# Performance work log

Hardware: AMD Instinct MI355X
Metric: run time of the kernel (lower is better)

The kernel has to match this reference:

```python
import jax, jax.numpy as jnp
import numpy as np

# Model constants (match init_kwargs and fla GatedLinearAttention defaults used in source)
L = 4            # num_layers
D = 1024         # d_model
H = 4            # n_heads
DK = 128         # head key dim  = 0.5*D / H
DV = 256         # head value dim = 1.0*D / H
KD = H * DK      # total key dim = 512
VD = H * DV      # total value dim = 1024
V = 32000        # vocab
B, T = 1, 2048
LR = 16          # gate_low_rank_dim
GLN = 16.0       # gate_logit_normalizer
EPS = 1e-5
SCALE = DK ** -0.5


def setup_inputs() -> dict:
    key = jax.random.key(0)
    ks = jax.random.split(key, 12)
    s = 0.02
    return {
        "input_ids": jax.random.randint(ks[0], (B, T), 0, V),
        "emb": jax.random.normal(ks[1], (V, D), jnp.float32) * s,
        "Wq": jax.random.normal(ks[2], (L, D, KD), jnp.float32) * s,
        "Wk": jax.random.normal(ks[3], (L, D, KD), jnp.float32) * s,
        "Wv": jax.random.normal(ks[4], (L, D, VD), jnp.float32) * s,
        "Wg": jax.random.normal(ks[5], (L, D, VD), jnp.float32) * s,
        "Wgk1": jax.random.normal(ks[6], (L, D, LR), jnp.float32) * s,
        "Wgk2": jax.random.normal(ks[7], (L, LR, KD), jnp.float32) * s,
        "bgk": jnp.zeros((L, KD), jnp.float32),
        "gnw": jnp.ones((L, DV), jnp.float32),
        "Wo": jax.random.normal(ks[8], (L, VD, D), jnp.float32) * s,
        "ln_w": jnp.ones((D,), jnp.float32),
        "ln_b": jnp.zeros((D,), jnp.float32),
        "Wlm": jax.random.normal(ks[9], (D, V), jnp.float32) * s,
        "blm": jnp.zeros((V,), jnp.float32),
    }


def _gla_layer(x, wq, wk, wv, wg, wg1, wg2, bg, nw, wo):
    # x: [B, T, D]
    b, t, _ = x.shape
    q = (x @ wq).reshape(b, t, H, DK) * SCALE
    k = (x @ wk).reshape(b, t, H, DK)
    v = (x @ wv).reshape(b, t, H, DV)
    g = (x @ wg).reshape(b, t, H, DV)
    # low-rank forget gate, log-space, normalized
    gk = (jax.nn.log_sigmoid((x @ wg1) @ wg2 + bg) / GLN).reshape(b, t, H, DK)

    # time-major for scan: [T, B, H, *]
    qt, kt, vt, gkt = (jnp.moveaxis(a, 1, 0) for a in (q, k, v, gk))

    def step(S, inp):
        q_t, k_t, v_t, gk_t = inp  # [B,H,DK], [B,H,DK], [B,H,DV], [B,H,DK]
        S = S * jnp.exp(gk_t)[..., None] + k_t[..., None] * v_t[..., None, :]
        o_t = jnp.einsum('bhk,bhkv->bhv', q_t, S)
        return S, o_t

    S0 = jnp.zeros((b, H, DK, DV), x.dtype)
    _, o = jax.lax.scan(step, S0, (qt, kt, vt, gkt))
    o = jnp.moveaxis(o, 0, 1)  # [B, T, H, DV]
    # fused RMSNorm + swish output gate
    o = o * jax.lax.rsqrt(jnp.mean(o * o, axis=-1, keepdims=True) + EPS) * nw
    o = o * (g * jax.nn.sigmoid(g))
    return o.reshape(b, t, VD) @ wo


def reference(input_ids, emb, Wq, Wk, Wv, Wg, Wgk1, Wgk2, bgk, gnw, Wo, ln_w, ln_b, Wlm, blm):
    h = emb[input_ids]  # [B, T, D]
    for i in range(L):
        h = _gla_layer(h, Wq[i], Wk[i], Wv[i], Wg[i], Wgk1[i], Wgk2[i], bgk[i], gnw[i], Wo[i])
    mu = jnp.mean(h, axis=-1, keepdims=True)
    var = jnp.mean((h - mu) ** 2, axis=-1, keepdims=True)
    h = (h - mu) * jax.lax.rsqrt(var + EPS) * ln_w + ln_b
    return h @ Wlm + blm
```

## Files before the change

kernel.cpp:

```cpp
#include <hip/hip_runtime.h>
#include <hip/hip_bf16.h>
#include <math.h>

#define NL 4
#define TT 2048
#define DD 1024
#define KDIM 512
#define VDIM 1024
#define QSTR 3072
#define NH 4
#define DKH 128
#define DVH 256
#define CH 64
#define NCH 32
#define VOCAB 32000
#define SCALE_Q 0.08838834764831845f

typedef short bf16x8 __attribute__((ext_vector_type(8)));
typedef float f32x4 __attribute__((ext_vector_type(4)));

__device__ __forceinline__ void gload_lds16(const void* g, void* l) {
    __builtin_amdgcn_global_load_lds((const __attribute__((address_space(1))) void*)g,
                                     (__attribute__((address_space(3))) void*)l, 16, 0, 0);
}

__device__ __forceinline__ void store_bf16x4(__hip_bfloat16* p, float a, float b, float c, float d) {
    union { __hip_bfloat16 h[4]; ushort4 v; } r;
    r.h[0] = __float2bfloat16(a); r.h[1] = __float2bfloat16(b);
    r.h[2] = __float2bfloat16(c); r.h[3] = __float2bfloat16(d);
    *(ushort4*)p = r.v;
}

__global__ __launch_bounds__(256) void embed_kernel(const int* __restrict__ ids,
                                                    const float* __restrict__ emb,
                                                    float* __restrict__ h,
                                                    __hip_bfloat16* __restrict__ hb) {
    int idx = blockIdx.x * 256 + threadIdx.x;
    int t = idx >> 8, c4 = idx & 255;
    float4 v = *(const float4*)(emb + (size_t)ids[t] * DD + c4 * 4);
    *(float4*)(h + (size_t)t * DD + c4 * 4) = v;
    store_bf16x4(hb + (size_t)t * DD + c4 * 4, v.x, v.y, v.z, v.w);
}

__global__ __launch_bounds__(256) void tconv_kernel(const float* __restrict__ in,
                                                    __hip_bfloat16* __restrict__ out,
                                                    int K, int N) {
    __shared__ float tle[64][65];
    const int n0 = blockIdx.x * 64, k0 = blockIdx.y * 64;
    const int tid = threadIdx.x;
    const int ty = tid >> 4, tx = tid & 15;
#pragma unroll
    for (int u = 0; u < 4; u++) {
        int r = ty + u * 16;
        float4 v = *(const float4*)(in + (size_t)(k0 + r) * N + n0 + tx * 4);
        tle[r][tx * 4 + 0] = v.x; tle[r][tx * 4 + 1] = v.y;
        tle[r][tx * 4 + 2] = v.z; tle[r][tx * 4 + 3] = v.w;
    }
    __syncthreads();
#pragma unroll
    for (int u = 0; u < 4; u++) {
        int nn = u * 16 + ty;
        store_bf16x4(out + (size_t)(n0 + nn) * K + k0 + tx * 4,
                     tle[tx * 4 + 0][nn], tle[tx * 4 + 1][nn],
                     tle[tx * 4 + 2][nn], tle[tx * 4 + 3][nn]);
    }
}

__global__ __launch_bounds__(256) void tconv_all_kernel(const float* __restrict__ Wq,
                                                        const float* __restrict__ Wk,
                                                        const float* __restrict__ Wv,
                                                        const float* __restrict__ Wg,
                                                        const float* __restrict__ Wo,
                                                        __hip_bfloat16* __restrict__ Wt4,
                                                        __hip_bfloat16* __restrict__ WoT4) {
    __shared__ float tle[64][65];
    int l = blockIdx.x >> 10;
    int b = blockIdx.x & 1023;
    const float* wq = Wq + (size_t)l * DD * KDIM;
    const float* wk = Wk + (size_t)l * DD * KDIM;
    const float* wv = Wv + (size_t)l * DD * VDIM;
    const float* wg = Wg + (size_t)l * DD * VDIM;
    const float* wo = Wo + (size_t)l * VDIM * DD;
    __hip_bfloat16* Wt  = Wt4  + (size_t)l * QSTR * DD;
    __hip_bfloat16* WoT = WoT4 + (size_t)l * DD * VDIM;
    const float* src; __hip_bfloat16* dst; int N, local;
    if (b < 128)      { src = wq; dst = Wt;                         N = 512;  local = b; }
    else if (b < 256) { src = wk; dst = Wt + (size_t)512 * 1024;    N = 512;  local = b - 128; }
    else if (b < 512) { src = wv; dst = Wt + (size_t)1024 * 1024;   N = 1024; local = b - 256; }
    else if (b < 768) { src = wg; dst = Wt + (size_t)2048 * 1024;   N = 1024; local = b - 512; }
    else              { src = wo; dst = WoT;                        N = 1024; local = b - 768; }
    int nbx = N >> 6;
    int n0 = (local % nbx) * 64, k0 = (local / nbx) * 64;
    const int tid = threadIdx.x;
    const int ty = tid >> 4, tx = tid & 15;
#pragma unroll
    for (int u = 0; u < 4; u++) {
        int r = ty + u * 16;
        float4 v = *(const float4*)(src + (size_t)(k0 + r) * N + n0 + tx * 4);
        tle[r][tx * 4 + 0] = v.x; tle[r][tx * 4 + 1] = v.y;
        tle[r][tx * 4 + 2] = v.z; tle[r][tx * 4 + 3] = v.w;
    }
    __syncthreads();
#pragma unroll
    for (int u = 0; u < 4; u++) {
        int nn = u * 16 + ty;
        store_bf16x4(dst + (size_t)(n0 + nn) * 1024 + k0 + tx * 4,
                     tle[tx * 4 + 0][nn], tle[tx * 4 + 1][nn],
                     tle[tx * 4 + 2][nn], tle[tx * 4 + 3][nn]);
    }
}

template<int NF>
__global__ __launch_bounds__(256) void gemm_bf16_db(const __hip_bfloat16* __restrict__ A,
                                                    const __hip_bfloat16* __restrict__ Bt,
                                                    const float* __restrict__ bias,
                                                    float* __restrict__ C,
                                                    __hip_bfloat16* __restrict__ Cb,
                                                    int M, int N, int K) {
    __shared__ short a_lds[2][128 * 32];
    __shared__ short b_lds[2][NF * 32 * 32];
    const int tid = threadIdx.x;
    const int wv = tid >> 6, lane = tid & 63;
    const int wr = wv >> 1, wc = wv & 1;
    const int nbx = gridDim.x;
    int wg = blockIdx.y * nbx + blockIdx.x;
    int cpx = (nbx * gridDim.y) >> 3;
    int swz = (wg & 7) * cpx + (wg >> 3);
    const int m0 = (swz % nbx) * 128, n0 = (swz / nbx) * (NF * 32);
    const int lr = lane & 15, lk = (lane >> 4) * 8;

    f32x4 acc[4][NF];
#pragma unroll
    for (int m = 0; m < 4; m++)
#pragma unroll
        for (int n = 0; n < NF; n++) acc[m][n] = (f32x4)(0.f);

    auto STAGE = [&](int buf, int k0) {
#pragma unroll
        for (int u = 0; u < 2; u++) {
            int s = wv * 128 + u * 64 + lane;
            int r = s >> 2, kc = (s & 3) * 8;
            gload_lds16(A + (size_t)(m0 + r) * K + k0 + kc,
                        &a_lds[buf][(wv * 128 + u * 64) * 8]);
        }
        if constexpr (NF == 4) {
#pragma unroll
            for (int u = 0; u < 2; u++) {
                int s = wv * 128 + u * 64 + lane;
                int r = s >> 2, kc = (s & 3) * 8;
                gload_lds16(Bt + (size_t)(n0 + r) * K + k0 + kc,
                            &b_lds[buf][(wv * 128 + u * 64) * 8]);
            }
        } else {
            int s = wv * 64 + lane;
            int r = s >> 2, kc = (s & 3) * 8;
            gload_lds16(Bt + (size_t)(n0 + r) * K + k0 + kc,
                        &b_lds[buf][(wv * 64) * 8]);
        }
    };
    auto COMPUTE = [&](int buf) {
        bf16x8 af[4], bfr[NF];
#pragma unroll
        for (int m = 0; m < 4; m++)
            af[m] = *(const bf16x8*)&a_lds[buf][(wr * 64 + m * 16 + lr) * 32 + lk];
#pragma unroll
        for (int n = 0; n < NF; n++)
            bfr[n] = *(const bf16x8*)&b_lds[buf][(wc * (NF * 16) + n * 16 + lr) * 32 + lk];
#pragma unroll
        for (int m = 0; m < 4; m++)
#pragma unroll
            for (int n = 0; n < NF; n++)
                acc[m][n] = __builtin_amdgcn_mfma_f32_16x16x32_bf16(af[m], bfr[n], acc[m][n], 0, 0, 0);
    };

    STAGE(0, 0);
    __syncthreads();
    int cur = 0;
    for (int k0 = 32; k0 < K; k0 += 32) {
        STAGE(cur ^ 1, k0);
        COMPUTE(cur);
        __syncthreads();
        cur ^= 1;
    }
    COMPUTE(cur);

    const int rbase = (lane >> 4) * 4;
#pragma unroll
    for (int n = 0; n < NF; n++) {
        int col = n0 + wc * (NF * 16) + n * 16 + lr;
        float bv = bias ? bias[col] : 0.f;
#pragma unroll
        for (int m = 0; m < 4; m++) {
            int row = m0 + wr * 64 + m * 16 + rbase;
#pragma unroll
            for (int r = 0; r < 4; r++) {
                float val = acc[m][n][r] + bv;
                C[(size_t)(row + r) * N + col] = val;
                if (Cb) Cb[(size_t)(row + r) * N + col] = __float2bfloat16(val);
            }
        }
    }
}

__device__ __forceinline__ void lm_stage(const __hip_bfloat16* src, int row0,
                                         char* dst, int kt32, int wv, int lane, int K) {
#pragma unroll
    for (int ii = 0; ii < 2; ii++) {
        int o = (wv * 2 + ii) * 1024;
        int ob = o + lane * 16;
        int lg = ob ^ (((ob >> 7) & 7) << 4);
        int row = lg >> 6;
        int ce = (lg & 63) >> 1;
        gload_lds16(src + (size_t)(row0 + row) * K + kt32 * 32 + ce, dst + o);
    }
}

__device__ __forceinline__ bf16x8 lm_frag(const char* sub, int row, int lk2) {
    int lg = ((row >> 1) << 7) + ((row & 1) << 6) + lk2;
    return *(const bf16x8*)(sub + (lg ^ (((row >> 1) & 7) << 4)));
}

template<int PT, bool LOADB, int VM>
__device__ __forceinline__ void lm_phase(const char* aT, const char* bT,
                                         const __hip_bfloat16* ssrc, int srow0,
                                         char* sdst, int skt32,
                                         bf16x8 (&bfr)[4][2], f32x4 (&acc)[8][4],
                                         int wr, int wc, int lr, int lk2,
                                         int wv, int lane, int K) {
    if constexpr (LOADB) {
#pragma unroll
        for (int n = 0; n < 4; n++)
#pragma unroll
            for (int ks = 0; ks < 2; ks++)
                bfr[n][ks] = lm_frag(bT + ks * 16384, wc * 64 + n * 16 + lr, lk2);
    }
    bf16x8 af[2][2];
#pragma unroll
    for (int mm = 0; mm < 2; mm++)
#pragma unroll
        for (int ks = 0; ks < 2; ks++)
            af[mm][ks] = lm_frag(aT + ks * 16384, wr * 128 + (2 * PT + mm) * 16 + lr, lk2);
    lm_stage(ssrc, srow0, sdst, skt32, wv, lane, K);
    asm volatile("s_barrier" ::: "memory");
    __builtin_amdgcn_s_setprio(1);
#pragma unroll
    for (int mm = 0; mm < 2; mm++)
#pragma unroll
        for (int n = 0; n < 4; n++) {
            acc[2 * PT + mm][n] = __builtin_amdgcn_mfma_f32_16x16x32_bf16(af[mm][0], bfr[n][0], acc[2 * PT + mm][n], 0, 0, 0);
            acc[2 * PT + mm][n] = __builtin_amdgcn_mfma_f32_16x16x32_bf16(af[mm][1], bfr[n][1], acc[2 * PT + mm][n], 0, 0, 0);
        }
    __builtin_amdgcn_s_setprio(0);
    if constexpr (VM == 4) asm volatile("s_waitcnt vmcnt(4)" ::: "memory");
    asm volatile("s_barrier" ::: "memory");
}

__global__ __launch_bounds__(512, 1) void gemm256_lm(const __hip_bfloat16* __restrict__ A,
                                                     const __hip_bfloat16* __restrict__ Bt,
                                                     const float* __restrict__ bias,
                                                     float* __restrict__ C,
                                                     int M, int N, int K) {
    extern __shared__ __align__(16) char smem[];
    char* sA0 = smem;
    char* sA1 = smem + 32768;
    char* sB0 = smem + 65536;
    char* sB1 = smem + 98304;
    const int tid = threadIdx.x;
    const int wv = tid >> 6, lane = tid & 63;
    const int wr = wv >> 2, wc = wv & 3;
    const int lr = lane & 15, lk2 = (lane >> 4) * 16;

    const int nbx = gridDim.x;
    int wg = blockIdx.y * nbx + blockIdx.x;
    int cpx = (nbx * gridDim.y) >> 3;
    int swz = (wg & 7) * cpx + (wg >> 3);
    const int m0 = (swz % nbx) * 256;
    const int n0 = (swz / nbx) * 256;

    f32x4 acc[8][4];
#pragma unroll
    for (int m = 0; m < 8; m++)
#pragma unroll
        for (int n = 0; n < 4; n++) acc[m][n] = (f32x4)(0.f);

    const int NTI = K / 64;
    const int NI  = NTI / 2;

    lm_stage(A,  m0, sA0 + 0,     0, wv, lane, K);
    lm_stage(A,  m0, sA0 + 16384, 1, wv, lane, K);
    lm_stage(Bt, n0, sB0 + 0,     0, wv, lane, K);
    lm_stage(Bt, n0, sB0 + 16384, 1, wv, lane, K);
    lm_stage(Bt, n0, sB1 + 0,     2, wv, lane, K);
    lm_stage(Bt, n0, sB1 + 16384, 3, wv, lane, K);
    asm volatile("s_waitcnt vmcnt(0)" ::: "memory");
    asm volatile("s_barrier" ::: "memory");

    for (int i = 0; i < NI; i++) {
        int tOdd = 2 * i + 1;
        int tE   = 2 * i + 2 < NTI ? 2 * i + 2 : NTI - 1;
        int tB3  = 2 * i + 3 < NTI ? 2 * i + 3 : NTI - 1;
        bf16x8 bfr[4][2];
        lm_phase<0, true , 0>(sA0, sB0, A,  m0, sA1 + 0,     2 * tOdd + 0, bfr, acc, wr, wc, lr, lk2, wv, lane, K);
        lm_phase<1, false, 0>(sA0, sB0, A,  m0, sA1 + 16384, 2 * tOdd + 1, bfr, acc, wr, wc, lr, lk2, wv, lane, K);
        lm_phase<2, false, 0>(sA0, sB0, Bt, n0, sB0 + 0,     2 * tE   + 0, bfr, acc, wr, wc, lr, lk2, wv, lane, K);
        lm_phase<3, false, 4>(sA0, sB0, Bt, n0, sB0 + 16384, 2 * tE   + 1, bfr, acc, wr, wc, lr, lk2, wv, lane, K);
        lm_phase<0, true , 0>(sA1, sB1, A,  m0, sA0 + 0,     2 * tE   + 0, bfr, acc, wr, wc, lr, lk2, wv, lane, K);
        lm_phase<1, false, 0>(sA1, sB1, A,  m0, sA0 + 16384, 2 * tE   + 1, bfr, acc, wr, wc, lr, lk2, wv, lane, K);
        lm_phase<2, false, 0>(sA1, sB1, Bt, n0, sB1 + 0,     2 * tB3  + 0, bfr, acc, wr, wc, lr, lk2, wv, lane, K);
        lm_phase<3, false, 4>(sA1, sB1, Bt, n0, sB1 + 16384, 2 * tB3  + 1, bfr, acc, wr, wc, lr, lk2, wv, lane, K);
    }

    const int r4 = (lane >> 4) * 4;
#pragma unroll
    for (int n = 0; n < 4; n++) {
        int col = n0 + wc * 64 + n * 16 + lr;
        float bv = bias ? bias[col] : 0.f;
#pragma unroll
        for (int m = 0; m < 8; m++) {
            int row = m0 + wr * 128 + m * 16 + r4;
#pragma unroll
            for (int r = 0; r < 4; r++)
                __builtin_nontemporal_store(acc[m][n][r] + bv,
                                            C + (size_t)(row + r) * N + col);
        }
    }
}

__global__ __launch_bounds__(256) void lowrank1_kernel(const float* __restrict__ h,
                                                       const float* __restrict__ W1,
                                                       float* __restrict__ xg) {
    int t = blockIdx.x;
    int tid = threadIdx.x;
    int j = tid & 15, ks = tid >> 4;
    const float* hr = h + (size_t)t * DD + ks * 64;
    const float* w = W1 + (size_t)(ks * 64) * 16 + j;
    float acc = 0.f;
#pragma unroll 8
    for (int kk = 0; kk < 64; kk++) acc = fmaf(hr[kk], w[kk * 16], acc);
    __shared__ float red[16][17];
    red[ks][j] = acc;
    __syncthreads();
    if (tid < 16) {
        float s = 0.f;
#pragma unroll
        for (int r = 0; r < 16; r++) s += red[r][tid];
        xg[t * 16 + tid] = s;
    }
}

__global__ __launch_bounds__(256) void gatefuse2_kernel(const float* __restrict__ qkvg,
                                                        const float* __restrict__ xg,
                                                        const float* __restrict__ W2,
                                                        const float* __restrict__ bg,
                                                        float* __restrict__ Gl,
                                                        __hip_bfloat16* __restrict__ qhB,
                                                        __hip_bfloat16* __restrict__ khB,
                                                        __hip_bfloat16* __restrict__ ktT) {
    __shared__ float w2s[16][64];
    __shared__ float xgs[64][16];
    __shared__ float part[4][64];
    const int tid = threadIdx.x;
    const int j = tid & 63, sg = tid >> 6;
    const int cg = blockIdx.x & 7, c = blockIdx.x >> 3;
    const int col = cg * 64 + j;
#pragma unroll
    for (int r = 0; r < 4; r++)
        w2s[sg * 4 + r][j] = W2[(size_t)(sg * 4 + r) * KDIM + col];
#pragma unroll
    for (int u = 0; u < 4; u++) {
        int id = u * 256 + tid;
        int t = id >> 4, r = id & 15;
        xgs[t][r] = xg[(size_t)(c * 64 + t) * 16 + r];
    }
    __syncthreads();
    const float bgv = bg[col];
    float ls[16];
    float partial = 0.f;
#pragma unroll
    for (int i = 0; i < 16; i++) {
        int t = sg * 16 + i;
        float s = bgv;
#pragma unroll
        for (int r = 0; r < 16; r++) s = fmaf(xgs[t][r], w2s[r][j], s);
        float v = (fminf(s, 0.f) - log1pf(expf(-fabsf(s)))) * (1.f / 16.f);
        ls[i] = v;
        partial += v;
    }
    part[sg][j] = partial;
    __syncthreads();
    float base = 0.f, total = 0.f;
#pragma unroll
    for (int r = 0; r < 4; r++) {
        float p = part[r][j];
        if (r < sg) base += p;
        total += p;
    }
    if (sg == 0) Gl[c * KDIM + col] = total;
    const float eGl = expf(total);
    const int hh = col >> 7, dk = col & 127;
    __hip_bfloat16 ktbuf[16];
    float G = base;
#pragma unroll
    for (int i = 0; i < 16; i++) {
        int t = c * 64 + sg * 16 + i;
        G += ls[i];
        const float* qp = qkvg + (size_t)t * QSTR + col;
        float qv = qp[0], kv = qp[512];
        qhB[(size_t)t * KDIM + col] = __float2bfloat16(qv * expf(G) * SCALE_Q);
        float khv = kv * expf(-G);
        khB[(size_t)t * KDIM + col] = __float2bfloat16(khv);
        ktbuf[i] = __float2bfloat16(khv * eGl);
    }
    __hip_bfloat16* kp = ktT + ((size_t)(c * NH + hh) * DKH + dk) * CH + sg * 16;
    *(uint4*)(kp + 0) = *(uint4*)&ktbuf[0];
    *(uint4*)(kp + 8) = *(uint4*)&ktbuf[8];
}

__global__ __launch_bounds__(256) void vtrans_kernel(const float* __restrict__ qkvg,
                                                     __hip_bfloat16* __restrict__ vT) {
    __shared__ float tle[64][65];
    int bid = blockIdx.x;
    int dvq = bid & 3, hh = (bid >> 2) & 3, c = bid >> 4;
    int tid = threadIdx.x, ty = tid >> 4, tx = tid & 15;
#pragma unroll
    for (int u = 0; u < 4; u++) {
        int r = u * 16 + ty;
        float4 v = *(const float4*)(qkvg + (size_t)(c * 64 + r) * QSTR + 1024 + hh * DVH + dvq * 64 + tx * 4);
        tle[r][tx * 4 + 0] = v.x; tle[r][tx * 4 + 1] = v.y;
        tle[r][tx * 4 + 2] = v.z; tle[r][tx * 4 + 3] = v.w;
    }
    __syncthreads();
    __hip_bfloat16* dst = vT + ((size_t)(c * NH + hh) * DVH + dvq * 64) * CH;
#pragma unroll
    for (int u = 0; u < 4; u++) {
        int dv = u * 16 + ty;
        store_bf16x4(dst + (size_t)dv * CH + tx * 4,
                     tle[tx * 4 + 0][dv], tle[tx * 4 + 1][dv],
                     tle[tx * 4 + 2][dv], tle[tx * 4 + 3][dv]);
    }
}

__global__ __launch_bounds__(256) void chunkU_mfma(const __hip_bfloat16* __restrict__ vT,
                                                   const __hip_bfloat16* __restrict__ ktT,
                                                   __hip_bfloat16* __restrict__ U) {
    const int ch = blockIdx.x;
    const __hip_bfloat16* Ap = vT + (size_t)ch * DVH * CH;
    const __hip_bfloat16* Bp = ktT + (size_t)ch * DKH * CH;
    __hip_bfloat16* Cp = U + (size_t)ch * DVH * DKH;
    const int tid = threadIdx.x, wv = tid >> 6, lane = tid & 63;
    const int wr = wv >> 1, wc = wv & 1;
    const int lr = lane & 15, lk = (lane >> 4) * 8;
    f32x4 acc[8][4];
#pragma unroll
    for (int m = 0; m < 8; m++)
#pragma unroll
        for (int n = 0; n < 4; n++) acc[m][n] = (f32x4)(0.f);
#pragma unroll
    for (int ks = 0; ks < 2; ks++) {
        bf16x8 a[8], b[4];
#pragma unroll
        for (int m = 0; m < 8; m++)
            a[m] = *(const bf16x8*)(Ap + (size_t)(wr * 128 + m * 16 + lr) * CH + ks * 32 + lk);
#pragma unroll
        for (int n = 0; n < 4; n++)
            b[n] = *(const bf16x8*)(Bp + (size_t)(wc * 64 + n * 16 + lr) * CH + ks * 32 + lk);
#pragma unroll
        for (int m = 0; m < 8; m++)
#pragma unroll
            for (int n = 0; n < 4; n++)
                acc[m][n] = __builtin_amdgcn_mfma_f32_16x16x32_bf16(a[m], b[n], acc[m][n], 0, 0, 0);
    }
    const int r4 = (lane >> 4) * 4;
#pragma unroll
    for (int m = 0; m < 8; m++)
#pragma unroll
        for (int n = 0; n < 4; n++)
#pragma unroll
            for (int r = 0; r < 4; r++)
                Cp[(size_t)(wr * 128 + m * 16 + r4 + r) * DKH + wc * 64 + n * 16 + lr] =
                    __float2bfloat16(acc[m][n][r]);
}

__global__ __launch_bounds__(256) void scan_states_kernel(__hip_bfloat16* __restrict__ U,
                                                          const float* __restrict__ Gl) {
    int idx = blockIdx.x * 256 + threadIdx.x;
    int hh = idx >> 15, dv = (idx >> 7) & 255, dk = idx & 127;
    int col = hh * DKH + dk;
    float s = 0.f;
    for (int c = 0; c < NCH; c++) {
        __hip_bfloat16* p = U + ((size_t)(c * NH + hh) * DVH + dv) * DKH + dk;
        float u = __bfloat162float(*p);
        *p = __float2bfloat16(s);
        s = s * expf(Gl[c * KDIM + col]) + u;
    }
}

__global__ __launch_bounds__(256) void attn_rms_mfma(const __hip_bfloat16* __restrict__ qhB,
                                                     const __hip_bfloat16* __restrict__ khB,
                                                     const __hip_bfloat16* __restrict__ vT,
                                                     const __hip_bfloat16* __restrict__ Ub,
                                                     const float* __restrict__ qkvg,
                                                     const float* __restrict__ nw,
                                                     __hip_bfloat16* __restrict__ obb) {
    __shared__ __hip_bfloat16 P[32 * 72];
    __shared__ float sums[32][2];
    const int bid = blockIdx.x;
    const int rh = bid & 1, hh = (bid >> 1) & 3, c = bid >> 3;
    const int t0 = c * CH;
    const int tid = threadIdx.x, wv = tid >> 6, lane = tid & 63;
    const int half = wv >> 1, rg = wv & 1;
    const int lr = lane & 15, lk = (lane >> 4) * 8;
    const int r4 = (lane >> 4) * 4;
    const int rr = rh * 32 + rg * 16;

    bf16x8 qf[4];
#pragma unroll
    for (int ks = 0; ks < 4; ks++)
        qf[ks] = *(const bf16x8*)(qhB + (size_t)(t0 + rr + lr) * KDIM + hh * DKH + ks * 32 + lk);

    if (half == 0) {
        f32x4 s[4];
#pragma unroll
        for (int n = 0; n < 4; n++) s[n] = (f32x4)(0.f);
#pragma unroll
        for (int n = 0; n < 4; n++)
#pragma unroll
            for (int ks = 0; ks < 4; ks++) {
                bf16x8 kf = *(const bf16x8*)(khB + (size_t)(t0 + n * 16 + lr) * KDIM + hh * DKH + ks * 32 + lk);
                s[n] = __builtin_amdgcn_mfma_f32_16x16x32_bf16(qf[ks], kf, s[n], 0, 0, 0);
            }
#pragma unroll
        for (int n = 0; n < 4; n++)
#pragma unroll
            for (int r = 0; r < 4; r++) {
                int i = rr + r4 + r, j = n * 16 + lr;
                float val = (j <= i) ? s[n][r] : 0.f;
                P[(rg * 16 + r4 + r) * 72 + j] = __float2bfloat16(val);
            }
    }
    __syncthreads();

    const __hip_bfloat16* vTp = vT + ((size_t)(c * NH + hh) * DVH + half * 128) * CH;
    const __hip_bfloat16* Ubp = Ub + ((size_t)(c * NH + hh) * DVH + half * 128) * DKH;
    bf16x8 pf[2];
#pragma unroll
    for (int ks = 0; ks < 2; ks++)
        pf[ks] = *(const bf16x8*)&P[(rg * 16 + lr) * 72 + ks * 32 + lk];

    f32x4 o[8];
#pragma unroll
    for (int n = 0; n < 8; n++) o[n] = (f32x4)(0.f);
#pragma unroll
    for (int n = 0; n < 8; n++) {
#pragma unroll
        for (int ks = 0; ks < 2; ks++) {
            bf16x8 vf = *(const bf16x8*)(vTp + (size_t)(n * 16 + lr) * CH + ks * 32 + lk);
            o[n] = __builtin_amdgcn_mfma_f32_16x16x32_bf16(pf[ks], vf, o[n], 0, 0, 0);
        }
#pragma unroll
        for (int ks = 0; ks < 4; ks++) {
            bf16x8 uf = *(const bf16x8*)(Ubp + (size_t)(n * 16 + lr) * DKH + ks * 32 + lk);
            o[n] = __builtin_amdgcn_mfma_f32_16x16x32_bf16(qf[ks], uf, o[n], 0, 0, 0);
        }
    }

    float part[4];
#pragma unroll
    for (int r = 0; r < 4; r++) {
        float p = 0.f;
#pragma unroll
        for (int n = 0; n < 8; n++) p = fmaf(o[n][r], o[n][r], p);
        part[r] = p;
    }
#pragma unroll
    for (int off = 1; off < 16; off <<= 1)
#pragma unroll
        for (int r = 0; r < 4; r++) part[r] += __shfl_xor(part[r], off);
    if (lr == 0)
#pragma unroll
        for (int r = 0; r < 4; r++) sums[rg * 16 + r4 + r][half] = part[r];
    __syncthreads();

#pragma unroll
    for (int r = 0; r < 4; r++) {
        int lrow = rg * 16 + r4 + r;
        int t = t0 + rh * 32 + lrow;
        float tot = sums[lrow][0] + sums[lrow][1];
        float rinv = rsqrtf(tot * (1.f / 256.f) + 1e-5f);
#pragma unroll
        for (int n = 0; n < 8; n++) {
            int col = half * 128 + n * 16 + lr;
            float gv = qkvg[(size_t)t * QSTR + 2048 + hh * DVH + col];
            float val = o[n][r] * rinv * nw[col] * (gv / (1.f + expf(-gv)));
            obb[(size_t)t * VDIM + hh * DVH + col] = __float2bfloat16(val);
        }
    }
}

__global__ __launch_bounds__(256) void ln_kernel(const float* __restrict__ h,
                                                 const float* __restrict__ w,
                                                 const float* __restrict__ b,
                                                 __hip_bfloat16* __restrict__ out16) {
    int t = blockIdx.x;
    int tid = threadIdx.x;
    float4 x = *(const float4*)(h + (size_t)t * DD + tid * 4);
    float s = x.x + x.y + x.z + x.w;
    float ss = x.x * x.x + x.y * x.y + x.z * x.z + x.w * x.w;
#pragma unroll
    for (int off = 32; off > 0; off >>= 1) {
        s += __shfl_xor(s, off);
        ss += __shfl_xor(ss, off);
    }
    __shared__ float rs[4], rss[4];
    int wv = tid >> 6;
    if ((tid & 63) == 0) { rs[wv] = s; rss[wv] = ss; }
    __syncthreads();
    s = rs[0] + rs[1] + rs[2] + rs[3];
    ss = rss[0] + rss[1] + rss[2] + rss[3];
    float mu = s * (1.f / 1024.f);
    float var = ss * (1.f / 1024.f) - mu * mu;
    float r = rsqrtf(var + 1e-5f);
    float4 wv4 = *(const float4*)(w + tid * 4);
    float4 bv4 = *(const float4*)(b + tid * 4);
    store_bf16x4(out16 + (size_t)t * DD + tid * 4,
                 (x.x - mu) * r * wv4.x + bv4.x,
                 (x.y - mu) * r * wv4.y + bv4.y,
                 (x.z - mu) * r * wv4.z + bv4.z,
                 (x.w - mu) * r * wv4.w + bv4.w);
}

extern "C" void kernel_launch(void* const* d_in, const int* in_sizes, int n_in,
                              void* d_out, int out_size, void* d_ws, size_t ws_size,
                              hipStream_t stream) {
    const int*   ids  = (const int*)d_in[0];
    const float* emb  = (const float*)d_in[1];
    const float* Wq   = (const float*)d_in[2];
    const float* Wk   = (const float*)d_in[3];
    const float* Wv   = (const float*)d_in[4];
    const float* Wg   = (const float*)d_in[5];
    const float* Wgk1 = (const float*)d_in[6];
    const float* Wgk2 = (const float*)d_in[7];
    const float* bgk  = (const float*)d_in[8];
    const float* gnw  = (const float*)d_in[9];
    const float* Wo   = (const float*)d_in[10];
    const float* lnw  = (const float*)d_in[11];
    const float* lnb  = (const float*)d_in[12];
    const float* Wlm  = (const float*)d_in[13];
    const float* blm  = (const float*)d_in[14];
    float* out = (float*)d_out;

    float* ws = (float*)d_ws;
    float* h    = ws; ws += (size_t)TT * DD;
    float* qkvg = ws; ws += (size_t)TT * QSTR;
    float* xg   = ws; ws += (size_t)TT * 16;
    float* Gl   = ws; ws += (size_t)NCH * KDIM;
    __hip_bfloat16* hb    = (__hip_bfloat16*)ws; ws += (size_t)TT * DD / 2;
    __hip_bfloat16* obb   = (__hip_bfloat16*)ws; ws += (size_t)TT * DD / 2;
    __hip_bfloat16* lnb16 = (__hip_bfloat16*)ws; ws += (size_t)TT * DD / 2;
    __hip_bfloat16* qhB   = (__hip_bfloat16*)ws; ws += (size_t)TT * KDIM / 2;
    __hip_bfloat16* khB   = (__hip_bfloat16*)ws; ws += (size_t)TT * KDIM / 2;
    __hip_bfloat16* ktT   = (__hip_bfloat16*)ws; ws += (size_t)NCH * NH * DKH * CH / 2;
    __hip_bfloat16* vT    = (__hip_bfloat16*)ws; ws += (size_t)NCH * NH * DVH * CH / 2;
    __hip_bfloat16* Ub    = (__hip_bfloat16*)ws; ws += (size_t)NCH * NH * DVH * DKH / 2;
    __hip_bfloat16* Wt4   = (__hip_bfloat16*)ws; ws += (size_t)NL * QSTR * DD / 2;
    __hip_bfloat16* WoT4  = (__hip_bfloat16*)ws; ws += (size_t)NL * DD * VDIM / 2;
    __hip_bfloat16* WlmT  = (__hip_bfloat16*)ws; ws += (size_t)VOCAB * DD / 2;

    hipFuncSetAttribute((const void*)gemm256_lm,
                        hipFuncAttributeMaxDynamicSharedMemorySize, 131072);

    embed_kernel<<<TT, 256, 0, stream>>>(ids, emb, h, hb);
    tconv_all_kernel<<<NL * 1024, 256, 0, stream>>>(Wq, Wk, Wv, Wg, Wo, Wt4, WoT4);
    tconv_kernel<<<dim3(VOCAB / 64, DD / 64), 256, 0, stream>>>(Wlm, WlmT, DD, VOCAB);

    for (int l = 0; l < NL; l++) {
        const float* w1 = Wgk1 + (size_t)l * DD * 16;
        const float* w2 = Wgk2 + (size_t)l * 16 * KDIM;
        const float* bg = bgk + (size_t)l * KDIM;
        const float* nw = gnw + (size_t)l * DVH;
        const __hip_bfloat16* Wt  = Wt4  + (size_t)l * QSTR * DD;
        const __hip_bfloat16* WoT = WoT4 + (size_t)l * DD * VDIM;

        gemm_bf16_db<4><<<dim3(TT / 128, QSTR / 128), 256, 0, stream>>>(hb, Wt, nullptr, qkvg, nullptr, TT, QSTR, DD);
        lowrank1_kernel<<<TT, 256, 0, stream>>>(h, w1, xg);
        gatefuse2_kernel<<<NCH * (KDIM / 64), 256, 0, stream>>>(qkvg, xg, w2, bg, Gl, qhB, khB, ktT);
        vtrans_kernel<<<NCH * NH * 4, 256, 0, stream>>>(qkvg, vT);
        chunkU_mfma<<<NCH * NH, 256, 0, stream>>>(vT, ktT, Ub);
        scan_states_kernel<<<NH * DVH * DKH / 256, 256, 0, stream>>>(Ub, Gl);
        attn_rms_mfma<<<NCH * NH * 2, 256, 0, stream>>>(qhB, khB, vT, Ub, qkvg, nw, obb);
        gemm_bf16_db<2><<<dim3(TT / 128, DD / 64), 256, 0, stream>>>(obb, WoT, nullptr, h, hb, TT, DD, VDIM);
    }

    ln_kernel<<<TT, 256, 0, stream>>>(h, lnw, lnb, lnb16);
    gemm256_lm<<<dim3(TT / 256, VOCAB / 256), 512, 131072, stream>>>(lnb16, WlmT, blm, out, TT, VOCAB, DD);
}
```

Baseline: 648.9 us.

## Coarsen LM-head GEMM phases, relax prologue wait, merge gate and V-transpose kernels

The LM-head GEMM's main loop now runs four phases per iteration instead of eight. Each phase computes four A sub-tiles and stages two K-slices, which halves the barrier count. The prologue waits until only four loads are outstanding instead of draining all of them. The output stores become plain stores rather than nontemporal ones. Separately, the gate-fusion and V-transpose kernels are merged into one launch that branches on block index, removing one launch per layer. This raises register pressure from more A fragments and changes the load/compute overlap, and the relaxed waitcnt relies on the order in which loads were issued.

```diff
diff --git a/kernel.cpp b/kernel.cpp
--- a/kernel.cpp
+++ b/kernel.cpp
@@ -220,13 +220,13 @@
     return *(const bf16x8*)(sub + (lg ^ (((row >> 1) & 7) << 4)));
 }
 
-template<int PT, bool LOADB, int VM>
-__device__ __forceinline__ void lm_phase(const char* aT, const char* bT,
-                                         const __hip_bfloat16* ssrc, int srow0,
-                                         char* sdst, int skt32,
-                                         bf16x8 (&bfr)[4][2], f32x4 (&acc)[8][4],
-                                         int wr, int wc, int lr, int lk2,
-                                         int wv, int lane, int K) {
+template<int QB, bool LOADB, int VM>
+__device__ __forceinline__ void lm_phase4(const char* aT, const char* bT,
+                                          const __hip_bfloat16* ssrc, int srow0,
+                                          char* sdst, int skt,
+                                          bf16x8 (&bfr)[4][2], f32x4 (&acc)[8][4],
+                                          int wr, int wc, int lr, int lk2,
+                                          int wv, int lane, int K) {
     if constexpr (LOADB) {
 #pragma unroll
         for (int n = 0; n < 4; n++)
@@ -234,21 +234,22 @@
             for (int ks = 0; ks < 2; ks++)
                 bfr[n][ks] = lm_frag(bT + ks * 16384, wc * 64 + n * 16 + lr, lk2);
     }
-    bf16x8 af[2][2];
-#pragma unroll
-    for (int mm = 0; mm < 2; mm++)
+    bf16x8 af[4][2];
+#pragma unroll
+    for (int mm = 0; mm < 4; mm++)
 #pragma unroll
         for (int ks = 0; ks < 2; ks++)
-            af[mm][ks] = lm_frag(aT + ks * 16384, wr * 128 + (2 * PT + mm) * 16 + lr, lk2);
-    lm_stage(ssrc, srow0, sdst, skt32, wv, lane, K);
+            af[mm][ks] = lm_frag(aT + ks * 16384, wr * 128 + (QB + mm) * 16 + lr, lk2);
+    lm_stage(ssrc, srow0, sdst + 0,     2 * skt + 0, wv, lane, K);
+    lm_stage(ssrc, srow0, sdst + 16384, 2 * skt + 1, wv, lane, K);
     asm volatile("s_barrier" ::: "memory");
     __builtin_amdgcn_s_setprio(1);
 #pragma unroll
-    for (int mm = 0; mm < 2; mm++)
+    for (int mm = 0; mm < 4; mm++)
 #pragma unroll
         for (int n = 0; n < 4; n++) {
-            acc[2 * PT + mm][n] = __builtin_amdgcn_mfma_f32_16x16x32_bf16(af[mm][0], bfr[n][0], acc[2 * PT + mm][n], 0, 0, 0);
-            acc[2 * PT + mm][n] = __builtin_amdgcn_mfma_f32_16x16x32_bf16(af[mm][1], bfr[n][1], acc[2 * PT + mm][n], 0, 0, 0);
+            acc[QB + mm][n] = __builtin_amdgcn_mfma_f32_16x16x32_bf16(af[mm][0], bfr[n][0], acc[QB + mm][n], 0, 0, 0);
+            acc[QB + mm][n] = __builtin_amdgcn_mfma_f32_16x16x32_bf16(af[mm][1], bfr[n][1], acc[QB + mm][n], 0, 0, 0);
         }
     __builtin_amdgcn_s_setprio(0);
     if constexpr (VM == 4) asm volatile("s_waitcnt vmcnt(4)" ::: "memory");
@@ -292,7 +293,7 @@
     lm_stage(Bt, n0, sB0 + 16384, 1, wv, lane, K);
     lm_stage(Bt, n0, sB1 + 0,     2, wv, lane, K);
     lm_stage(Bt, n0, sB1 + 16384, 3, wv, lane, K);
-    asm volatile("s_waitcnt vmcnt(0)" ::: "memory");
+    asm volatile("s_waitcnt vmcnt(4)" ::: "memory");
     asm volatile("s_barrier" ::: "memory");
 
     for (int i = 0; i < NI; i++) {
@@ -300,14 +301,10 @@
         int tE   = 2 * i + 2 < NTI ? 2 * i + 2 : NTI - 1;
         int tB3  = 2 * i + 3 < NTI ? 2 * i + 3 : NTI - 1;
         bf16x8 bfr[4][2];
-        lm_phase<0, true , 0>(sA0, sB0, A,  m0, sA1 + 0,     2 * tOdd + 0, bfr, acc, wr, wc, lr, lk2, wv, lane, K);
-        lm_phase<1, false, 0>(sA0, sB0, A,  m0, sA1 + 16384, 2 * tOdd + 1, bfr, acc, wr, wc, lr, lk2, wv, lane, K);
-        lm_phase<2, false, 0>(sA0, sB0, Bt, n0, sB0 + 0,     2 * tE   + 0, bfr, acc, wr, wc, lr, lk2, wv, lane, K);
-        lm_phase<3, false, 4>(sA0, sB0, Bt, n0, sB0 + 16384, 2 * tE   + 1, bfr, acc, wr, wc, lr, lk2, wv, lane, K);
-        lm_phase<0, true , 0>(sA1, sB1, A,  m0, sA0 + 0,     2 * tE   + 0, bfr, acc, wr, wc, lr, lk2, wv, lane, K);
-        lm_phase<1, false, 0>(sA1, sB1, A,  m0, sA0 + 16384, 2 * tE   + 1, bfr, acc, wr, wc, lr, lk2, wv, lane, K);
-        lm_phase<2, false, 0>(sA1, sB1, Bt, n0, sB1 + 0,     2 * tB3  + 0, bfr, acc, wr, wc, lr, lk2, wv, lane, K);
-        lm_phase<3, false, 4>(sA1, sB1, Bt, n0, sB1 + 16384, 2 * tB3  + 1, bfr, acc, wr, wc, lr, lk2, wv, lane, K);
+        lm_phase4<0, true , 0>(sA0, sB0, A,  m0, sA1, tOdd, bfr, acc, wr, wc, lr, lk2, wv, lane, K);
+        lm_phase4<4, false, 4>(sA0, sB0, Bt, n0, sB0, tE,   bfr, acc, wr, wc, lr, lk2, wv, lane, K);
+        lm_phase4<0, true , 0>(sA1, sB1, A,  m0, sA0, tE,   bfr, acc, wr, wc, lr, lk2, wv, lane, K);
+        lm_phase4<4, false, 4>(sA1, sB1, Bt, n0, sB1, tB3,  bfr, acc, wr, wc, lr, lk2, wv, lane, K);
     }
 
     const int r4 = (lane >> 4) * 4;
@@ -320,8 +317,7 @@
             int row = m0 + wr * 128 + m * 16 + r4;
 #pragma unroll
             for (int r = 0; r < 4; r++)
-                __builtin_nontemporal_store(acc[m][n][r] + bv,
-                                            C + (size_t)(row + r) * N + col);
+                C[(size_t)(row + r) * N + col] = acc[m][n][r] + bv;
         }
     }
 }
@@ -348,95 +344,96 @@
     }
 }
 
-__global__ __launch_bounds__(256) void gatefuse2_kernel(const float* __restrict__ qkvg,
-                                                        const float* __restrict__ xg,
-                                                        const float* __restrict__ W2,
-                                                        const float* __restrict__ bg,
-                                                        float* __restrict__ Gl,
-                                                        __hip_bfloat16* __restrict__ qhB,
-                                                        __hip_bfloat16* __restrict__ khB,
-                                                        __hip_bfloat16* __restrict__ ktT) {
-    __shared__ float w2s[16][64];
-    __shared__ float xgs[64][16];
-    __shared__ float part[4][64];
+__global__ __launch_bounds__(256) void gatevt_kernel(const float* __restrict__ qkvg,
+                                                     const float* __restrict__ xg,
+                                                     const float* __restrict__ W2,
+                                                     const float* __restrict__ bg,
+                                                     float* __restrict__ Gl,
+                                                     __hip_bfloat16* __restrict__ qhB,
+                                                     __hip_bfloat16* __restrict__ khB,
+                                                     __hip_bfloat16* __restrict__ ktT,
+                                                     __hip_bfloat16* __restrict__ vT) {
+    __shared__ __align__(16) char smemc[64 * 65 * 4];
     const int tid = threadIdx.x;
-    const int j = tid & 63, sg = tid >> 6;
-    const int cg = blockIdx.x & 7, c = blockIdx.x >> 3;
-    const int col = cg * 64 + j;
-#pragma unroll
-    for (int r = 0; r < 4; r++)
-        w2s[sg * 4 + r][j] = W2[(size_t)(sg * 4 + r) * KDIM + col];
-#pragma unroll
-    for (int u = 0; u < 4; u++) {
-        int id = u * 256 + tid;
-        int t = id >> 4, r = id & 15;
-        xgs[t][r] = xg[(size_t)(c * 64 + t) * 16 + r];
-    }
-    __syncthreads();
-    const float bgv = bg[col];
-    float ls[16];
-    float partial = 0.f;
-#pragma unroll
-    for (int i = 0; i < 16; i++) {
-        int t = sg * 16 + i;
-        float s = bgv;
-#pragma unroll
-        for (int r = 0; r < 16; r++) s = fmaf(xgs[t][r], w2s[r][j], s);
-        float v = (fminf(s, 0.f) - log1pf(expf(-fabsf(s)))) * (1.f / 16.f);
-        ls[i] = v;
-        partial += v;
-    }
-    part[sg][j] = partial;
-    __syncthreads();
-    float base = 0.f, total = 0.f;
-#pragma unroll
-    for (int r = 0; r < 4; r++) {
-        float p = part[r][j];
-        if (r < sg) base += p;
-        total += p;
-    }
-    if (sg == 0) Gl[c * KDIM + col] = total;
-    const float eGl = expf(total);
-    const int hh = col >> 7, dk = col & 127;
-    __hip_bfloat16 ktbuf[16];
-    float G = base;
-#pragma unroll
-    for (int i = 0; i < 16; i++) {
-        int t = c * 64 + sg * 16 + i;
-        G += ls[i];
-        const float* qp = qkvg + (size_t)t * QSTR + col;
-        float qv = qp[0], kv = qp[512];
-        qhB[(size_t)t * KDIM + col] = __float2bfloat16(qv * expf(G) * SCALE_Q);
-        float khv = kv * expf(-G);
-        khB[(size_t)t * KDIM + col] = __float2bfloat16(khv);
-        ktbuf[i] = __float2bfloat16(khv * eGl);
-    }
-    __hip_bfloat16* kp = ktT + ((size_t)(c * NH + hh) * DKH + dk) * CH + sg * 16;
-    *(uint4*)(kp + 0) = *(uint4*)&ktbuf[0];
-    *(uint4*)(kp + 8) = *(uint4*)&ktbuf[8];
-}
-
-__global__ __launch_bounds__(256) void vtrans_kernel(const float* __restrict__ qkvg,
-                                                     __hip_bfloat16* __restrict__ vT) {
-    __shared__ float tle[64][65];
-    int bid = blockIdx.x;
-    int dvq = bid & 3, hh = (bid >> 2) & 3, c = bid >> 4;
-    int tid = threadIdx.x, ty = tid >> 4, tx = tid & 15;
-#pragma unroll
-    for (int u = 0; u < 4; u++) {
-        int r = u * 16 + ty;
-        float4 v = *(const float4*)(qkvg + (size_t)(c * 64 + r) * QSTR + 1024 + hh * DVH + dvq * 64 + tx * 4);
-        tle[r][tx * 4 + 0] = v.x; tle[r][tx * 4 + 1] = v.y;
-        tle[r][tx * 4 + 2] = v.z; tle[r][tx * 4 + 3] = v.w;
-    }
-    __syncthreads();
-    __hip_bfloat16* dst = vT + ((size_t)(c * NH + hh) * DVH + dvq * 64) * CH;
-#pragma unroll
-    for (int u = 0; u < 4; u++) {
-        int dv = u * 16 + ty;
-        store_bf16x4(dst + (size_t)dv * CH + tx * 4,
-                     tle[tx * 4 + 0][dv], tle[tx * 4 + 1][dv],
-                     tle[tx * 4 + 2][dv], tle[tx * 4 + 3][dv]);
+    if (blockIdx.x < 256) {
+        float (*w2s)[64] = (float(*)[64])smemc;
+        float (*xgs)[16] = (float(*)[16])(smemc + 4096);
+        float (*part)[64] = (float(*)[64])(smemc + 8192);
+        const int j = tid & 63, sg = tid >> 6;
+        const int cg = blockIdx.x & 7, c = blockIdx.x >> 3;
+        const int col = cg * 64 + j;
+#pragma unroll
+        for (int r = 0; r < 4; r++)
+            w2s[sg * 4 + r][j] = W2[(size_t)(sg * 4 + r) * KDIM + col];
+#pragma unroll
+        for (int u = 0; u < 4; u++) {
+            int id = u * 256 + tid;
+            int t = id >> 4, r = id & 15;
+            xgs[t][r] = xg[(size_t)(c * 64 + t) * 16 + r];
+        }
+        __syncthreads();
+        const float bgv = bg[col];
+        float ls[16];
+        float partial = 0.f;
+#pragma unroll
+        for (int i = 0; i < 16; i++) {
+            int t = sg * 16 + i;
+            float s = bgv;
+#pragma unroll
+            for (int r = 0; r < 16; r++) s = fmaf(xgs[t][r], w2s[r][j], s);
+            float v = (fminf(s, 0.f) - log1pf(expf(-fabsf(s)))) * (1.f / 16.f);
+            ls[i] = v;
+            partial += v;
+        }
+        part[sg][j] = partial;
+        __syncthreads();
+        float base = 0.f, total = 0.f;
+#pragma unroll
+        for (int r = 0; r < 4; r++) {
+            float p = part[r][j];
+            if (r < sg) base += p;
+            total += p;
+        }
+        if (sg == 0) Gl[c * KDIM + col] = total;
+        const float eGl = expf(total);
+        const int hh = col >> 7, dk = col & 127;
+        __hip_bfloat16 ktbuf[16];
+        float G = base;
+#pragma unroll
+        for (int i = 0; i < 16; i++) {
+            int t = c * 64 + sg * 16 + i;
+            G += ls[i];
+            const float* qp = qkvg + (size_t)t * QSTR + col;
+            float qv = qp[0], kv = qp[512];
+            qhB[(size_t)t * KDIM + col] = __float2bfloat16(qv * expf(G) * SCALE_Q);
+            float khv = kv * expf(-G);
+            khB[(size_t)t * KDIM + col] = __float2bfloat16(khv);
+            ktbuf[i] = __float2bfloat16(khv * eGl);
+        }
+        __hip_bfloat16* kp = ktT + ((size_t)(c * NH + hh) * DKH + dk) * CH + sg * 16;
+        *(uint4*)(kp + 0) = *(uint4*)&ktbuf[0];
+        *(uint4*)(kp + 8) = *(uint4*)&ktbuf[8];
+    } else {
+        float (*tle)[65] = (float(*)[65])smemc;
+        int bid = blockIdx.x - 256;
+        int dvq = bid & 3, hh = (bid >> 2) & 3, c = bid >> 4;
+        int ty = tid >> 4, tx = tid & 15;
+#pragma unroll
+        for (int u = 0; u < 4; u++) {
+            int r = u * 16 + ty;
+            float4 v = *(const float4*)(qkvg + (size_t)(c * 64 + r) * QSTR + 1024 + hh * DVH + dvq * 64 + tx * 4);
+            tle[r][tx * 4 + 0] = v.x; tle[r][tx * 4 + 1] = v.y;
+            tle[r][tx * 4 + 2] = v.z; tle[r][tx * 4 + 3] = v.w;
+        }
+        __syncthreads();
+        __hip_bfloat16* dst = vT + ((size_t)(c * NH + hh) * DVH + dvq * 64) * CH;
+#pragma unroll
+        for (int u = 0; u < 4; u++) {
+            int dv = u * 16 + ty;
+            store_bf16x4(dst + (size_t)dv * CH + tx * 4,
+                         tle[tx * 4 + 0][dv], tle[tx * 4 + 1][dv],
+                         tle[tx * 4 + 2][dv], tle[tx * 4 + 3][dv]);
+        }
     }
 }
 
@@ -683,8 +680,7 @@
 
         gemm_bf16_db<4><<<dim3(TT / 128, QSTR / 128), 256, 0, stream>>>(hb, Wt, nullptr, qkvg, nullptr, TT, QSTR, DD);
         lowrank1_kernel<<<TT, 256, 0, stream>>>(h, w1, xg);
-        gatefuse2_kernel<<<NCH * (KDIM / 64), 256, 0, stream>>>(qkvg, xg, w2, bg, Gl, qhB, khB, ktT);
-        vtrans_kernel<<<NCH * NH * 4, 256, 0, stream>>>(qkvg, vT);
+        gatevt_kernel<<<768, 256, 0, stream>>>(qkvg, xg, w2, bg, Gl, qhB, khB, ktT, vT);
         chunkU_mfma<<<NCH * NH, 256, 0, stream>>>(vT, ktT, Ub);
         scan_states_kernel<<<NH * DVH * DKH / 256, 256, 0, stream>>>(Ub, Gl);
         attn_rms_mfma<<<NCH * NH * 2, 256, 0, stream>>>(qhB, khB, vT, Ub, qkvg, nw, obb);
```

After: 685.9 us. +5.7%, slower.
